# Performance work log

Measured on AMD Instinct MI355X. Metric: run time of the kernel, lower is better.

The kernel has to match this reference:

```python
import jax, jax.numpy as jnp
import numpy as np

B, RES, DIM, H, KD = 16, 32, 768, 12, 64
N = RES * RES          # 1024 tokens
D = KD                 # attn_ratio = 1 -> per-head value dim == key_dim
DH = D * H             # 768
SCALE = KD ** -0.5
LN_EPS = 1e-5


def _bias_idxs():
    # replicate the itertools.product construction: for row-major points,
    # offsets (|dy|,|dx|) are first seen in order dy-major, so id = |dy|*RES + |dx|
    coords = np.arange(N)
    y, x = coords // RES, coords % RES
    dy = np.abs(y[:, None] - y[None, :])
    dx = np.abs(x[:, None] - x[None, :])
    return jnp.asarray(dy * RES + dx, dtype=jnp.int32)  # [N, N]


def setup_inputs() -> dict:
    key = jax.random.key(0)
    ks = jax.random.split(key, 8)
    return {
        "x": jax.random.normal(ks[0], (B, N, DIM), jnp.float32),
        "ln_w": 1.0 + 0.01 * jax.random.normal(ks[1], (DIM,), jnp.float32),
        "ln_b": 0.01 * jax.random.normal(ks[2], (DIM,), jnp.float32),
        "qkv_w": 0.02 * jax.random.normal(ks[3], (3 * H * KD, DIM), jnp.float32),
        "qkv_b": 0.01 * jax.random.normal(ks[4], (3 * H * KD,), jnp.float32),
        "proj_w": 0.02 * jax.random.normal(ks[5], (DIM, DH), jnp.float32),
        "proj_b": 0.01 * jax.random.normal(ks[6], (DIM,), jnp.float32),
        "attn_biases": 0.1 * jax.random.normal(ks[7], (H, RES * RES), jnp.float32),
        "bias_idxs": _bias_idxs(),
    }


def reference(x, ln_w, ln_b, qkv_w, qkv_b, proj_w, proj_b, attn_biases, bias_idxs):
    # LayerNorm over the feature dim
    mu = jnp.mean(x, axis=-1, keepdims=True)
    var = jnp.mean(jnp.square(x - mu), axis=-1, keepdims=True)
    xn = (x - mu) * jax.lax.rsqrt(var + LN_EPS) * ln_w + ln_b

    # fused qkv projection -> [B, N, H, 3*KD], split per head
    qkv = (xn @ qkv_w.T + qkv_b).reshape(B, N, H, 3 * KD)
    q, k, v = jnp.split(qkv, [KD, 2 * KD], axis=3)  # each [B, N, H, KD]

    # gathered relative-position bias: [H, N, N]
    bias = attn_biases[:, bias_idxs]

    # scores + bias -> softmax -> AV
    attn = jnp.einsum("bnhk,bmhk->bhnm", q, k) * SCALE + bias[None]
    attn = jax.nn.softmax(attn, axis=-1)
    out = jnp.einsum("bhnm,bmhd->bnhd", attn, v).reshape(B, N, DH)
    return out @ proj_w.T + proj_b
```

## Files before the change

### kernel.cpp

```cpp
#include <hip/hip_runtime.h>
#include <cstdint>
#include <cstddef>

#define AS1 __attribute__((address_space(1)))
#define AS3 __attribute__((address_space(3)))

typedef float f32x4 __attribute__((ext_vector_type(4)));
typedef __bf16 bf16x8 __attribute__((ext_vector_type(8)));
typedef __bf16 bf16x4 __attribute__((ext_vector_type(4)));
typedef uint32_t u32x4 __attribute__((ext_vector_type(4)));

__device__ __forceinline__ void async_cp16(void* lds, const void* g) {
    __builtin_amdgcn_global_load_lds((AS1 void*)(g), (AS3 void*)(lds), 16, 0, 0);
}

__device__ __forceinline__ bf16x8 frag_of(u32x4 u) {
    return __builtin_bit_cast(bf16x8, u);
}

__global__ __launch_bounds__(256)
void cvt_w(const float* __restrict__ qkvw, const float* __restrict__ projw,
           __bf16* __restrict__ qkvwb, __bf16* __restrict__ projwb) {
    int i = blockIdx.x * 256 + threadIdx.x;
    if (i < 442368) {
        int row = i / 192, c4 = (i - row * 192) * 4;
        int t = (row >= 1536) ? 2 : (row >= 768 ? 1 : 0);
        int rem = row - t * 768;
        int hh = rem >> 6, d = rem & 63;
        int in_row = hh * 192 + t * 64 + d;
        float4 v = *(const float4*)(qkvw + (long)in_row * 768 + c4);
        bf16x4 o;
        o[0] = (__bf16)v.x; o[1] = (__bf16)v.y; o[2] = (__bf16)v.z; o[3] = (__bf16)v.w;
        *(bf16x4*)(qkvwb + (long)row * 768 + c4) = o;
    } else {
        int j = i - 442368;
        float4 v = ((const float4*)projw)[j];
        bf16x4 o;
        o[0] = (__bf16)v.x; o[1] = (__bf16)v.y; o[2] = (__bf16)v.z; o[3] = (__bf16)v.w;
        ((bf16x4*)projwb)[j] = o;
    }
}

__global__ __launch_bounds__(256)
void ln_kernel(const float* __restrict__ x, const float* __restrict__ w,
               const float* __restrict__ bsh, __bf16* __restrict__ xn) {
    const int lane = threadIdx.x & 63;
    const long row = (long)blockIdx.x * 4 + (threadIdx.x >> 6);
    const float4* xr = (const float4*)(x + row * 768);
    float4 v[3];
    v[0] = xr[lane]; v[1] = xr[lane + 64]; v[2] = xr[lane + 128];
    float s = 0.f, ss = 0.f;
#pragma unroll
    for (int i = 0; i < 3; ++i) {
        s  += v[i].x + v[i].y + v[i].z + v[i].w;
        ss += v[i].x * v[i].x + v[i].y * v[i].y + v[i].z * v[i].z + v[i].w * v[i].w;
    }
#pragma unroll
    for (int m = 1; m < 64; m <<= 1) { s += __shfl_xor(s, m); ss += __shfl_xor(ss, m); }
    const float mean = s * (1.f / 768.f);
    const float rstd = rsqrtf(ss * (1.f / 768.f) - mean * mean + 1e-5f);
    const float4* wv = (const float4*)w;
    const float4* bv = (const float4*)bsh;
    bf16x4* outp = (bf16x4*)(xn + row * 768);
#pragma unroll
    for (int i = 0; i < 3; ++i) {
        float4 wi = wv[lane + 64 * i], bi = bv[lane + 64 * i];
        bf16x4 o;
        o[0] = (__bf16)((v[i].x - mean) * rstd * wi.x + bi.x);
        o[1] = (__bf16)((v[i].y - mean) * rstd * wi.y + bi.y);
        o[2] = (__bf16)((v[i].z - mean) * rstd * wi.z + bi.z);
        o[3] = (__bf16)((v[i].w - mean) * rstd * wi.w + bi.w);
        outp[lane + 64 * i] = o;
    }
}

template <int MODE>
__device__ __forceinline__
void gemm_core(char* smem,
               const __bf16* __restrict__ A, const __bf16* __restrict__ Bw,
               const float* __restrict__ bias,
               __bf16* __restrict__ q_out, __bf16* __restrict__ k_out,
               __bf16* __restrict__ vt_out, float* __restrict__ f_out,
               long bm, long bn) {
    constexpr int K = 768;
    const int tid  = threadIdx.x;
    const int lane = tid & 63;
    const int quad = lane >> 4;
    const int l16  = lane & 15;
    const int wave = tid >> 6;
    const int wm = wave >> 1, wn = wave & 1;

    const __bf16* Ab = A  + bm * K;
    const __bf16* Bb = Bw + bn * K;

    const int e0 = tid, e1 = tid + 256;
    const int rA0 = e0 >> 2, c0 = ((e0 & 3) ^ ((e0 >> 3) & 3)) * 8;
    const int rA1 = e1 >> 2, c1 = ((e1 & 3) ^ ((e1 >> 3) & 3)) * 8;
    const int swq = quad ^ ((l16 >> 1) & 3);

    f32x4 acc[4][4] = {};

    auto stage = [&](int t) {
        char* base = smem + (t % 3) * 16384;
        const __bf16* As_ = Ab + t * 32;
        const __bf16* Bs_ = Bb + t * 32;
        async_cp16(base + e0 * 16,        As_ + (long)rA0 * K + c0);
        async_cp16(base + e1 * 16,        As_ + (long)rA1 * K + c1);
        async_cp16(base + 8192 + e0 * 16, Bs_ + (long)rA0 * K + c0);
        async_cp16(base + 8192 + e1 * 16, Bs_ + (long)rA1 * K + c1);
    };

    auto kstep = [&](int buf) {
        const u32x4* Av = (const u32x4*)(smem + buf * 16384);
        const u32x4* Bv = (const u32x4*)(smem + buf * 16384 + 8192);
        bf16x8 af[4], bfr[4];
#pragma unroll
        for (int t = 0; t < 4; ++t) {
            af[t]  = frag_of(Av[(wm * 64 + t * 16 + l16) * 4 + swq]);
            bfr[t] = frag_of(Bv[(wn * 64 + t * 16 + l16) * 4 + swq]);
        }
        __builtin_amdgcn_s_setprio(1);
#pragma unroll
        for (int i = 0; i < 4; ++i)
#pragma unroll
            for (int j = 0; j < 4; ++j) {
                if constexpr (MODE == 0)
                    acc[i][j] = __builtin_amdgcn_mfma_f32_16x16x32_bf16(bfr[j], af[i], acc[i][j], 0, 0, 0);
                else
                    acc[i][j] = __builtin_amdgcn_mfma_f32_16x16x32_bf16(af[i], bfr[j], acc[i][j], 0, 0, 0);
            }
        __builtin_amdgcn_s_setprio(0);
    };

    stage(0); stage(1);
    for (int t = 0; t < 23; ++t) {
        asm volatile("s_waitcnt vmcnt(4)" ::: "memory");
        __builtin_amdgcn_s_barrier();
        if (t < 22) stage(t + 2);
        kstep(t % 3);
    }
    asm volatile("s_waitcnt vmcnt(0)" ::: "memory");
    __builtin_amdgcn_s_barrier();
    kstep(23 % 3);

    if constexpr (MODE == 0) {
#pragma unroll
        for (int j = 0; j < 4; ++j) {
            int col0 = (int)bn + wn * 64 + j * 16 + quad * 4;
            int t  = col0 >= 768;
            int cc = col0 - t * 768;
            int h  = cc >> 6, d = cc & 63;
            int f  = h * 192 + t * 64 + d;
            float4 bb = *(const float4*)(bias + f);
            __bf16* dst = t ? k_out : q_out;
#pragma unroll
            for (int i = 0; i < 4; ++i) {
                long row = bm + wm * 64 + i * 16 + l16;
                long b   = row >> 10;
                long n   = row & 1023;
                bf16x4 pk;
                pk[0] = (__bf16)(acc[i][j][0] + bb.x);
                pk[1] = (__bf16)(acc[i][j][1] + bb.y);
                pk[2] = (__bf16)(acc[i][j][2] + bb.z);
                pk[3] = (__bf16)(acc[i][j][3] + bb.w);
                *(bf16x4*)(dst + ((b * 12 + h) * 1024 + n) * 64 + d) = pk;
            }
        }
    } else if constexpr (MODE == 2) {
#pragma unroll
        for (int j = 0; j < 4; ++j) {
            int cv = (int)bn - 1536 + wn * 64 + j * 16 + l16;
            int h  = cv >> 6, d = cv & 63;
            float bv = bias[h * 192 + 128 + d];
#pragma unroll
            for (int i = 0; i < 4; ++i) {
                long row0 = bm + wm * 64 + i * 16 + quad * 4;
                long b    = row0 >> 10;
                long n0   = row0 & 1023;
                bf16x4 pk;
                pk[0] = (__bf16)(acc[i][j][0] + bv);
                pk[1] = (__bf16)(acc[i][j][1] + bv);
                pk[2] = (__bf16)(acc[i][j][2] + bv);
                pk[3] = (__bf16)(acc[i][j][3] + bv);
                *(bf16x4*)(vt_out + ((b * 12 + h) * 64 + d) * 1024 + n0) = pk;
            }
        }
    } else {
#pragma unroll
        for (int i = 0; i < 4; ++i) {
#pragma unroll
            for (int r = 0; r < 4; ++r) {
                long row = bm + wm * 64 + i * 16 + quad * 4 + r;
#pragma unroll
                for (int j = 0; j < 4; ++j) {
                    int col = (int)bn + wn * 64 + j * 16 + l16;
                    f_out[row * 768 + col] = acc[i][j][r] + bias[col];
                }
            }
        }
    }
}

__global__ __launch_bounds__(256, 3)
void gemm_qkv(const __bf16* __restrict__ A, const __bf16* __restrict__ Bw,
              const float* __restrict__ bias, __bf16* __restrict__ qb,
              __bf16* __restrict__ kb, __bf16* __restrict__ vtb) {
    __shared__ __align__(16) char smem[49152];
    int blk  = blockIdx.x;
    int xcd  = blk & 7;
    int rest = blk >> 3;
    int bx   = rest % 18;
    int byg  = rest / 18;
    long by  = xcd + 8 * byg;
    if (bx < 12)
        gemm_core<0>(smem, A, Bw, bias, qb, kb, nullptr, nullptr, by * 128, (long)bx * 128);
    else
        gemm_core<2>(smem, A, Bw, bias, nullptr, nullptr, vtb, nullptr, by * 128, (long)bx * 128);
}

__global__ __launch_bounds__(256, 3)
void gemm_proj(const __bf16* __restrict__ A, const __bf16* __restrict__ Bw,
               const float* __restrict__ bias, float* __restrict__ out) {
    __shared__ __align__(16) char smem[49152];
    int blk  = blockIdx.x;
    int xcd  = blk & 7;
    int rest = blk >> 3;
    int bx   = rest % 6;
    int byg  = rest / 6;
    long by  = xcd + 8 * byg;
    gemm_core<1>(smem, A, Bw, bias, nullptr, nullptr, nullptr, out,
                 by * 128, (long)bx * 128);
}

__global__ __launch_bounds__(256, 4)
void attn_kernel(const __bf16* __restrict__ Q, const __bf16* __restrict__ Kb,
                 const __bf16* __restrict__ Vt, const float* __restrict__ biases,
                 __bf16* __restrict__ out) {
    __shared__ __align__(16) __bf16 Ks[2][64 * 64];
    __shared__ __align__(16) __bf16 Vts[2][64 * 64];
    __shared__ __align__(16) float brow[1024];

    const int tid  = threadIdx.x;
    const int lane = tid & 63;
    const int wave = tid >> 6;
    const int quad = lane >> 4;
    const int l16  = lane & 15;
    const int sw   = l16 & 7;

    int blk  = blockIdx.x;
    int xcd  = blk & 7;
    int rest = blk >> 3;
    int qt   = rest & 7;
    int bhg  = rest >> 3;
    int bh_i = xcd + 8 * bhg;
    int b    = bh_i / 12;
    int h    = bh_i - b * 12;

    const long bh = bh_i;
    const __bf16* Qg  = Q  + (bh * 1024 + qt * 128) * 64;
    const __bf16* Kg  = Kb + bh * 1024 * 64;
    const __bf16* Vtg = Vt + bh * 64 * 1024;

    const int rk = tid >> 3;
    const int ck = (tid & 7) ^ (rk & 7);

    {
        const float LOG2E = 1.4426950408889634f;
        float4 v = ((const float4*)(biases + (long)h * 1024))[tid];
        float4 o; o.x = v.x * LOG2E; o.y = v.y * LOG2E;
        o.z = v.z * LOG2E; o.w = v.w * LOG2E;
        *(float4*)(brow + tid * 4) = o;
    }
#pragma unroll
    for (int j = 0; j < 4; ++j) {
        int e = tid + 256 * j;
        int r = e >> 3, c = (e & 7) ^ (r & 7);
        async_cp16((char*)Vts + e * 16, Qg + r * 64 + c * 8);
    }
    async_cp16((char*)Ks[0] + tid * 16,         Kg + rk * 64 + ck * 8);
    async_cp16((char*)Ks[0] + (tid + 256) * 16, Kg + (rk + 32) * 64 + ck * 8);
    __syncthreads();

    bf16x8 aq[2][2];
    {
        const u32x4* Qv = (const u32x4*)Vts;
#pragma unroll
        for (int g = 0; g < 2; ++g) {
            int qrow = wave * 32 + g * 16 + l16;
            aq[g][0] = frag_of(Qv[qrow * 8 + (quad ^ sw)]);
            aq[g][1] = frag_of(Qv[qrow * 8 + ((quad + 4) ^ sw)]);
        }
    }
    __syncthreads();
    async_cp16((char*)Vts[0] + tid * 16,         Vtg + rk * 1024 + ck * 8);
    async_cp16((char*)Vts[0] + (tid + 256) * 16, Vtg + (rk + 32) * 1024 + ck * 8);
    __syncthreads();

    const int yq = 4 * qt + wave;
    int pdx00[4], pdx01[4], pdx10[4];
#pragma unroll
    for (int r = 0; r < 4; ++r) {
        int xk = quad * 4 + r;
        int d0 = l16 - xk;
        pdx00[r] = d0 < 0 ? -d0 : d0;
        pdx01[r] = 16 - d0;
        pdx10[r] = 16 + d0;
    }

    const float SSCALE = 0.125f * 1.4426950408889634f;
    float lacc[2] = {0.f, 0.f};
    f32x4 o[2][4] = {};
    const int q2 = quad >> 1;
    const int hb = (quad & 1) * 8;

    for (int kt = 0; kt < 16; ++kt) {
        const int cb = kt & 1;
        if (kt < 15) {
            const int nb = cb ^ 1;
            const __bf16* Kt  = Kg  + (kt + 1) * 4096;
            const __bf16* Vtt = Vtg + (kt + 1) * 64;
            async_cp16((char*)Ks[nb]  + tid * 16,         Kt  + rk * 64 + ck * 8);
            async_cp16((char*)Ks[nb]  + (tid + 256) * 16, Kt  + (rk + 32) * 64 + ck * 8);
            async_cp16((char*)Vts[nb] + tid * 16,         Vtt + rk * 1024 + ck * 8);
            async_cp16((char*)Vts[nb] + (tid + 256) * 16, Vtt + (rk + 32) * 1024 + ck * 8);
        }

        f32x4 s[2][4];
        const u32x4* Kv = (const u32x4*)Ks[cb];
#pragma unroll
        for (int nt = 0; nt < 4; ++nt) {
            int krow = nt * 16 + l16;
            bf16x8 k0 = frag_of(Kv[krow * 8 + (quad ^ sw)]);
            bf16x8 k1 = frag_of(Kv[krow * 8 + ((quad + 4) ^ sw)]);
#pragma unroll
            for (int g = 0; g < 2; ++g) {
                f32x4 z = {0.f, 0.f, 0.f, 0.f};
                z = __builtin_amdgcn_mfma_f32_16x16x32_bf16(k0, aq[g][0], z, 0, 0, 0);
                z = __builtin_amdgcn_mfma_f32_16x16x32_bf16(k1, aq[g][1], z, 0, 0, 0);
                s[g][nt] = z;
            }
        }

        int dy0 = yq - 2 * kt;     dy0 = dy0 < 0 ? -dy0 : dy0;
        int dy1 = yq - 2 * kt - 1; dy1 = dy1 < 0 ? -dy1 : dy1;
        const float* br0 = brow + dy0 * 32;
        const float* br1 = brow + dy1 * 32;

        bf16x8 bpA[2], bpB[2];
#pragma unroll
        for (int g = 0; g < 2; ++g) {
#pragma unroll
            for (int nt = 0; nt < 4; ++nt) {
                const float* br = (nt & 2) ? br1 : br0;
#pragma unroll
                for (int r = 0; r < 4; ++r) {
                    int idx = (nt & 1) ? (g ? pdx00[r] : pdx01[r])
                                       : (g ? pdx10[r] : pdx00[r]);
                    float p = __builtin_amdgcn_exp2f(s[g][nt][r] * SSCALE + br[idx]);
                    lacc[g] += p;
                    if (nt < 2) bpA[g][(nt & 1) * 4 + r] = (__bf16)p;
                    else        bpB[g][(nt & 1) * 4 + r] = (__bf16)p;
                }
            }
        }

        const char* Vb = (const char*)Vts[cb];
#pragma unroll
        for (int dt = 0; dt < 4; ++dt) {
            int rb = (dt * 16 + l16) * 128 + hb;
            uint2 alo = *(const uint2*)(Vb + rb + (((q2    ) ^ sw) << 4));
            uint2 ahi = *(const uint2*)(Vb + rb + (((q2 + 2) ^ sw) << 4));
            uint2 blo = *(const uint2*)(Vb + rb + (((q2 + 4) ^ sw) << 4));
            uint2 bhi = *(const uint2*)(Vb + rb + (((q2 + 6) ^ sw) << 4));
            u32x4 va = {alo.x, alo.y, ahi.x, ahi.y};
            u32x4 vbk = {blo.x, blo.y, bhi.x, bhi.y};
            bf16x8 vA = frag_of(va), vB = frag_of(vbk);
#pragma unroll
            for (int g = 0; g < 2; ++g) {
                o[g][dt] = __builtin_amdgcn_mfma_f32_16x16x32_bf16(vA, bpA[g], o[g][dt], 0, 0, 0);
                o[g][dt] = __builtin_amdgcn_mfma_f32_16x16x32_bf16(vB, bpB[g], o[g][dt], 0, 0, 0);
            }
        }

        __syncthreads();
    }

#pragma unroll
    for (int g = 0; g < 2; ++g) {
        float la = lacc[g];
        la += __shfl_xor(la, 16);
        la += __shfl_xor(la, 32);
        const float rl = 1.f / la;
        const long n = qt * 128 + wave * 32 + g * 16 + l16;
        __bf16* op = out + ((long)b * 1024 + n) * 768 + h * 64 + quad * 4;
#pragma unroll
        for (int dt = 0; dt < 4; ++dt) {
            bf16x4 ov;
            ov[0] = (__bf16)(o[g][dt][0] * rl);
            ov[1] = (__bf16)(o[g][dt][1] * rl);
            ov[2] = (__bf16)(o[g][dt][2] * rl);
            ov[3] = (__bf16)(o[g][dt][3] * rl);
            *(bf16x4*)(op + dt * 16) = ov;
        }
    }
}

extern "C" void kernel_launch(void* const* d_in, const int* in_sizes, int n_in,
                              void* d_out, int out_size, void* d_ws, size_t ws_size,
                              hipStream_t stream) {
    (void)in_sizes; (void)n_in; (void)out_size; (void)ws_size;
    const float* x      = (const float*)d_in[0];
    const float* ln_w   = (const float*)d_in[1];
    const float* ln_b   = (const float*)d_in[2];
    const float* qkv_w  = (const float*)d_in[3];
    const float* qkv_b  = (const float*)d_in[4];
    const float* proj_w = (const float*)d_in[5];
    const float* proj_b = (const float*)d_in[6];
    const float* ab     = (const float*)d_in[7];
    float* outp = (float*)d_out;

    char* ws = (char*)d_ws;
    __bf16* xn     = (__bf16*)(ws);
    __bf16* aout   = (__bf16*)(ws);
    __bf16* qkvwb  = (__bf16*)(ws + 25165824);
    __bf16* projwb = (__bf16*)(ws + 28704768);
    __bf16* qb     = (__bf16*)(ws + 29884416);
    __bf16* kb     = (__bf16*)(ws + 55050240);
    __bf16* vtb    = (__bf16*)(ws + 80216064);

    cvt_w<<<2304, 256, 0, stream>>>(qkv_w, proj_w, qkvwb, projwb);
    ln_kernel<<<4096, 256, 0, stream>>>(x, ln_w, ln_b, xn);
    gemm_qkv<<<2304, 256, 0, stream>>>(xn, qkvwb, qkv_b, qb, kb, vtb);
    attn_kernel<<<1536, 256, 0, stream>>>(qb, kb, vtb, ab, aout);
    gemm_proj<<<768, 256, 0, stream>>>(aout, projwb, proj_b, outp);
}
```

Measured before the change: 323.7 us.

## Shrink attention key tile to 32 and route P through per-wave LDS

The attention kernel now processes 32 keys per iteration instead of 64, which halves the K/V double-buffer footprint and packs everything into one 28KB shared buffer. The probability tile is written to a per-wave LDS scratch and read back as full 16-byte fragments, so the V fragments no longer have to be gathered with four 8-byte reads. The intent is lower LDS use for better occupancy and fewer fragment shuffles. In exchange there are twice as many loop iterations and barriers, plus an extra LDS write/read round trip for P.

Measured after the change: 298.7 us. 7.7% less time.

```diff
diff --git a/kernel.cpp b/kernel.cpp
--- a/kernel.cpp
+++ b/kernel.cpp
@@ -236,9 +236,8 @@
 void attn_kernel(const __bf16* __restrict__ Q, const __bf16* __restrict__ Kb,
                  const __bf16* __restrict__ Vt, const float* __restrict__ biases,
                  __bf16* __restrict__ out) {
-    __shared__ __align__(16) __bf16 Ks[2][64 * 64];
-    __shared__ __align__(16) __bf16 Vts[2][64 * 64];
-    __shared__ __align__(16) float brow[1024];
+    __shared__ __align__(16) char smem[28672];
+    float* brow = (float*)(smem + 24576);
 
     const int tid  = threadIdx.x;
     const int lane = tid & 63;
@@ -246,6 +245,7 @@
     const int quad = lane >> 4;
     const int l16  = lane & 15;
     const int sw   = l16 & 7;
+    const int swp  = (l16 >> 1) & 3;
 
     int blk  = blockIdx.x;
     int xcd  = blk & 7;
@@ -263,27 +263,27 @@
 
     const int rk = tid >> 3;
     const int ck = (tid & 7) ^ (rk & 7);
+    const int rv = tid >> 2;
+    const int cv = (tid & 3) ^ ((tid >> 3) & 3);
 
     {
         const float LOG2E = 1.4426950408889634f;
         float4 v = ((const float4*)(biases + (long)h * 1024))[tid];
         float4 o; o.x = v.x * LOG2E; o.y = v.y * LOG2E;
         o.z = v.z * LOG2E; o.w = v.w * LOG2E;
-        *(float4*)(brow + tid * 4) = o;
+        ((float4*)brow)[tid] = o;
     }
 #pragma unroll
     for (int j = 0; j < 4; ++j) {
         int e = tid + 256 * j;
         int r = e >> 3, c = (e & 7) ^ (r & 7);
-        async_cp16((char*)Vts + e * 16, Qg + r * 64 + c * 8);
-    }
-    async_cp16((char*)Ks[0] + tid * 16,         Kg + rk * 64 + ck * 8);
-    async_cp16((char*)Ks[0] + (tid + 256) * 16, Kg + (rk + 32) * 64 + ck * 8);
+        async_cp16(smem + e * 16, Qg + r * 64 + c * 8);
+    }
     __syncthreads();
 
     bf16x8 aq[2][2];
     {
-        const u32x4* Qv = (const u32x4*)Vts;
+        const u32x4* Qv = (const u32x4*)smem;
 #pragma unroll
         for (int g = 0; g < 2; ++g) {
             int qrow = wave * 32 + g * 16 + l16;
@@ -292,16 +292,15 @@
         }
     }
     __syncthreads();
-    async_cp16((char*)Vts[0] + tid * 16,         Vtg + rk * 1024 + ck * 8);
-    async_cp16((char*)Vts[0] + (tid + 256) * 16, Vtg + (rk + 32) * 1024 + ck * 8);
+    async_cp16(smem + tid * 16,        Kg  + rk * 64   + ck * 8);
+    async_cp16(smem + 8192 + tid * 16, Vtg + rv * 1024 + cv * 8);
     __syncthreads();
 
     const int yq = 4 * qt + wave;
     int pdx00[4], pdx01[4], pdx10[4];
 #pragma unroll
     for (int r = 0; r < 4; ++r) {
-        int xk = quad * 4 + r;
-        int d0 = l16 - xk;
+        int d0 = l16 - (quad * 4 + r);
         pdx00[r] = d0 < 0 ? -d0 : d0;
         pdx01[r] = 16 - d0;
         pdx10[r] = 16 + d0;
@@ -310,25 +309,24 @@
     const float SSCALE = 0.125f * 1.4426950408889634f;
     float lacc[2] = {0.f, 0.f};
     f32x4 o[2][4] = {};
-    const int q2 = quad >> 1;
+    char* Pw = smem + 16384 + wave * 2048;
     const int hb = (quad & 1) * 8;
-
-    for (int kt = 0; kt < 16; ++kt) {
+    const int pslotw = (quad >> 1);
+
+    for (int kt = 0; kt < 32; ++kt) {
         const int cb = kt & 1;
-        if (kt < 15) {
+        if (kt < 31) {
             const int nb = cb ^ 1;
-            const __bf16* Kt  = Kg  + (kt + 1) * 4096;
-            const __bf16* Vtt = Vtg + (kt + 1) * 64;
-            async_cp16((char*)Ks[nb]  + tid * 16,         Kt  + rk * 64 + ck * 8);
-            async_cp16((char*)Ks[nb]  + (tid + 256) * 16, Kt  + (rk + 32) * 64 + ck * 8);
-            async_cp16((char*)Vts[nb] + tid * 16,         Vtt + rk * 1024 + ck * 8);
-            async_cp16((char*)Vts[nb] + (tid + 256) * 16, Vtt + (rk + 32) * 1024 + ck * 8);
-        }
-
-        f32x4 s[2][4];
-        const u32x4* Kv = (const u32x4*)Ks[cb];
-#pragma unroll
-        for (int nt = 0; nt < 4; ++nt) {
+            async_cp16(smem + nb * 4096 + tid * 16,
+                       Kg + (kt + 1) * 2048 + rk * 64 + ck * 8);
+            async_cp16(smem + 8192 + nb * 4096 + tid * 16,
+                       Vtg + (kt + 1) * 32 + rv * 1024 + cv * 8);
+        }
+
+        f32x4 s[2][2];
+        const u32x4* Kv = (const u32x4*)(smem + cb * 4096);
+#pragma unroll
+        for (int nt = 0; nt < 2; ++nt) {
             int krow = nt * 16 + l16;
             bf16x8 k0 = frag_of(Kv[krow * 8 + (quad ^ sw)]);
             bf16x8 k1 = frag_of(Kv[krow * 8 + ((quad + 4) ^ sw)]);
@@ -341,45 +339,36 @@
             }
         }
 
-        int dy0 = yq - 2 * kt;     dy0 = dy0 < 0 ? -dy0 : dy0;
-        int dy1 = yq - 2 * kt - 1; dy1 = dy1 < 0 ? -dy1 : dy1;
-        const float* br0 = brow + dy0 * 32;
-        const float* br1 = brow + dy1 * 32;
-
-        bf16x8 bpA[2], bpB[2];
+        int dyv = yq - kt; dyv = dyv < 0 ? -dyv : dyv;
+        const float* br = brow + dyv * 32;
 #pragma unroll
         for (int g = 0; g < 2; ++g) {
 #pragma unroll
-            for (int nt = 0; nt < 4; ++nt) {
-                const float* br = (nt & 2) ? br1 : br0;
+            for (int nt = 0; nt < 2; ++nt) {
+                const int* pdx = (g == nt) ? pdx00 : (g ? pdx10 : pdx01);
+                bf16x4 pk;
 #pragma unroll
                 for (int r = 0; r < 4; ++r) {
-                    int idx = (nt & 1) ? (g ? pdx00[r] : pdx01[r])
-                                       : (g ? pdx10[r] : pdx00[r]);
-                    float p = __builtin_amdgcn_exp2f(s[g][nt][r] * SSCALE + br[idx]);
+                    float p = __builtin_amdgcn_exp2f(s[g][nt][r] * SSCALE + br[pdx[r]]);
                     lacc[g] += p;
-                    if (nt < 2) bpA[g][(nt & 1) * 4 + r] = (__bf16)p;
-                    else        bpB[g][(nt & 1) * 4 + r] = (__bf16)p;
+                    pk[r] = (__bf16)p;
                 }
-            }
-        }
-
-        const char* Vb = (const char*)Vts[cb];
+                int slot = (nt * 2 + pslotw) ^ swp;
+                *(bf16x4*)(Pw + (g * 16 + l16) * 64 + slot * 16 + hb) = pk;
+            }
+        }
+
+        bf16x8 bp[2];
+#pragma unroll
+        for (int g = 0; g < 2; ++g)
+            bp[g] = frag_of(*(const u32x4*)(Pw + (g * 16 + l16) * 64 + ((quad ^ swp) << 4)));
+        const char* Vb = smem + 8192 + cb * 4096;
 #pragma unroll
         for (int dt = 0; dt < 4; ++dt) {
-            int rb = (dt * 16 + l16) * 128 + hb;
-            uint2 alo = *(const uint2*)(Vb + rb + (((q2    ) ^ sw) << 4));
-            uint2 ahi = *(const uint2*)(Vb + rb + (((q2 + 2) ^ sw) << 4));
-            uint2 blo = *(const uint2*)(Vb + rb + (((q2 + 4) ^ sw) << 4));
-            uint2 bhi = *(const uint2*)(Vb + rb + (((q2 + 6) ^ sw) << 4));
-            u32x4 va = {alo.x, alo.y, ahi.x, ahi.y};
-            u32x4 vbk = {blo.x, blo.y, bhi.x, bhi.y};
-            bf16x8 vA = frag_of(va), vB = frag_of(vbk);
-#pragma unroll
-            for (int g = 0; g < 2; ++g) {
-                o[g][dt] = __builtin_amdgcn_mfma_f32_16x16x32_bf16(vA, bpA[g], o[g][dt], 0, 0, 0);
-                o[g][dt] = __builtin_amdgcn_mfma_f32_16x16x32_bf16(vB, bpB[g], o[g][dt], 0, 0, 0);
-            }
+            bf16x8 vf = frag_of(*(const u32x4*)(Vb + (dt * 16 + l16) * 64 + ((quad ^ swp) << 4)));
+#pragma unroll
+            for (int g = 0; g < 2; ++g)
+                o[g][dt] = __builtin_amdgcn_mfma_f32_16x16x32_bf16(vf, bp[g], o[g][dt], 0, 0, 0);
         }
 
         __syncthreads();
```
